# Kernel optimization log

Measured on AMD Instinct MI355X. Metric: run time of the kernel, lower is better.

## Reference

```python
import jax, jax.numpy as jnp
import numpy as np


def topk_sparsify(x, k):
    # keep k entries with largest |x|, zero the rest (matches TopKFunction.forward)
    _, idx = jax.lax.top_k(jnp.abs(x), k)            # [B, k]
    vals = jnp.take_along_axis(x, idx, axis=-1)      # [B, k]
    out = jnp.zeros_like(x)
    b = jnp.arange(x.shape[0])[:, None]              # [B, 1]
    return out.at[b, idx].set(vals)


def setup_inputs() -> dict:
    key = jax.random.key(0)
    k1, k2, k3 = jax.random.split(key, 3)
    B, D, L = 4096, 768, 16384
    x = jax.random.normal(k1, (B, D), dtype=jnp.float32)
    # kaiming_normal_(fan_out) -> std = sqrt(2 / latent_dim); then *= 2.0
    enc_w = jax.random.normal(k2, (L, D), dtype=jnp.float32) * (2.0 * np.sqrt(2.0 / L))
    enc_b = jnp.zeros((L,), dtype=jnp.float32)
    # torch Linear default init: uniform(-1/sqrt(fan_in), 1/sqrt(fan_in))
    bound = 1.0 / np.sqrt(L)
    dec_w = jax.random.uniform(k3, (D, L), dtype=jnp.float32, minval=-bound, maxval=bound)
    dec_b = jnp.zeros((D,), dtype=jnp.float32)
    return {"x": x, "enc_w": enc_w, "enc_b": enc_b, "dec_w": dec_w, "dec_b": dec_b, "k": 32}


def reference(x, enc_w, enc_b, dec_w, dec_b, k):
    pre = x @ enc_w.T + enc_b            # [B, L]
    latents = topk_sparsify(pre, k)      # [B, L], k-sparse per row
    recon = latents @ dec_w.T + dec_b    # [B, D]
    return (recon, latents, pre)
```

## Files before the change

### kernel.cpp

```cpp
#include <hip/hip_runtime.h>
#include <hip/hip_bf16.h>
#include <stdint.h>


typedef __attribute__((ext_vector_type(8))) short bf16x8;
typedef __attribute__((ext_vector_type(4))) float f32x4;

__device__ __forceinline__ ushort f2bf_rne(float v) {
    unsigned u = __float_as_uint(v);
    return (ushort)((u + 0x7fffu + ((u >> 16) & 1u)) >> 16);
}
__device__ __forceinline__ float bf2f(ushort h) {
    return __uint_as_float(((unsigned)h) << 16);
}

__global__ __launch_bounds__(256)
void prep_all(const float* __restrict__ x, const float* __restrict__ enc_w,
              const float* __restrict__ dec_w,
              ushort* __restrict__ Ah, ushort* __restrict__ Wh,
              ushort* __restrict__ WTb,
              int nA, int nW, int KT, int K, int D, int L)
{
    __shared__ float tile[32][33];
    const int bid = blockIdx.x;
    if (bid < nA + nW) {
        const float* X;
        ushort* P;
        int base;
        if (bid < nA) { X = x;     P = Ah; base = bid; }
        else          { X = enc_w; P = Wh; base = bid - nA; }
        int t = base * 256 + threadIdx.x;
        int lane = t & 63;
        int rest = t >> 6;
        int r16 = rest / KT, kt = rest - r16 * KT;
        int row = (r16 << 4) + (lane & 15);
        int k0  = (kt << 5) + ((lane >> 4) << 3);
        const float* src = X + (size_t)row * K + k0;
        uint hw[4];
        #pragma unroll
        for (int i = 0; i < 4; ++i) {
            float v0 = src[2 * i], v1 = src[2 * i + 1];
            hw[i] = (uint)f2bf_rne(v0) | ((uint)f2bf_rne(v1) << 16);
        }
        *reinterpret_cast<uint4*>(P + (size_t)t * 8) = make_uint4(hw[0], hw[1], hw[2], hw[3]);
    } else {
        int tb = bid - nA - nW;
        int gx = L >> 5;
        int l0 = (tb % gx) << 5;
        int d0 = (tb / gx) << 5;
        int tx = threadIdx.x & 31;
        int ty = threadIdx.x >> 5;
        for (int i = ty; i < 32; i += 8)
            tile[i][tx] = dec_w[(size_t)(d0 + i) * L + (l0 + tx)];
        __syncthreads();
        for (int i = ty; i < 32; i += 8)
            WTb[(size_t)(l0 + i) * D + (d0 + tx)] = f2bf_rne(tile[tx][i]);
    }
}

__global__ __launch_bounds__(256, 4)
void encoder_mfma1(const ushort* __restrict__ Ah, const ushort* __restrict__ Wh,
                   const float* __restrict__ bias, float* __restrict__ C,
                   int M, int N, int K)
{
    __shared__ ushort lds[2][8192];
    const int KT = K >> 5;
    const int tid  = threadIdx.x;
    const int lane = tid & 63;
    const int wid  = tid >> 6;

    const int gy    = M >> 7;
    const int rpx   = gy >> 3;
    const int xcd   = blockIdx.x & 7;
    const int local = blockIdx.x >> 3;
    const int by    = xcd * rpx + (local % rpx);
    const int bx    = local / rpx;

    const int wr = wid >> 1, wc = wid & 1;

    f32x4 acc[4][4];
    #pragma unroll
    for (int m = 0; m < 4; ++m)
        #pragma unroll
        for (int n = 0; n < 4; ++n) acc[m][n] = (f32x4){0.f, 0.f, 0.f, 0.f};

    auto STAGE = [&](int buf, int kt) {
        #pragma unroll
        for (int c0 = 0; c0 < 4; ++c0) {
            int c   = (wid << 2) + c0;
            int fr  = c & 7;
            int rb  = ((c < 8) ? (by << 3) : (bx << 3)) + fr;
            const ushort* g = ((c < 8) ? Ah : Wh) + (((size_t)rb * KT + kt) * 64 + lane) * 8;
            ushort* dst = &lds[buf][c * 512];
            __builtin_amdgcn_global_load_lds(
                (const __attribute__((address_space(1))) unsigned int*)g,
                (__attribute__((address_space(3))) unsigned int*)dst, 16, 0, 0);
        }
    };

    STAGE(0, 0);
    __syncthreads();

    int cur = 0;
    for (int kt = 0; kt < KT; ++kt) {
        if (kt + 1 < KT) STAGE(cur ^ 1, kt + 1);

        bf16x8 ah[4], bh[4];
        #pragma unroll
        for (int m = 0; m < 4; ++m)
            ah[m] = *reinterpret_cast<const bf16x8*>(&lds[cur][((wr << 2) + m) * 512 + lane * 8]);
        #pragma unroll
        for (int n = 0; n < 4; ++n)
            bh[n] = *reinterpret_cast<const bf16x8*>(&lds[cur][4096 + ((wc << 2) + n) * 512 + lane * 8]);

        #pragma unroll
        for (int m = 0; m < 4; ++m)
            #pragma unroll
            for (int n = 0; n < 4; ++n)
                acc[m][n] = __builtin_amdgcn_mfma_f32_16x16x32_bf16(ah[m], bh[n], acc[m][n], 0, 0, 0);

        __syncthreads();
        cur ^= 1;
    }

    const int r_in = (lane >> 4) << 2;
    const int c_in = lane & 15;
    #pragma unroll
    for (int n = 0; n < 4; ++n) {
        const int gc = (bx << 7) + (wc << 6) + (n << 4) + c_in;
        const float bv = bias[gc];
        #pragma unroll
        for (int m = 0; m < 4; ++m) {
            const int gr0 = (by << 7) + (wr << 6) + (m << 4) + r_in;
            #pragma unroll
            for (int q = 0; q < 4; ++q)
                __builtin_nontemporal_store(acc[m][n][q] + bv,
                                            &C[(size_t)(gr0 + q) * N + gc]);
        }
    }
}

#define SR_CAP 1024
#define SR_ZCAP 128

__global__ __launch_bounds__(256, 8)
void select_refine(const float* __restrict__ pre, const float* __restrict__ x,
                   const float* __restrict__ enc_w, const float* __restrict__ enc_b,
                   float* __restrict__ latents, int* __restrict__ sel_idx,
                   float* __restrict__ sel_val, const int* __restrict__ kptr,
                   const ushort* __restrict__ WT, const float* __restrict__ dbias,
                   float* __restrict__ recon, int D, int L)
{
    const int b   = blockIdx.x;
    const int tid = threadIdx.x;
    const float* row = pre + (size_t)b * L;
    float* lrow = latents + (size_t)b * L;

    __shared__ float    xs[768];
    __shared__ float    smp[256];
    __shared__ float    sthr[3];
    __shared__ int      cnt;
    __shared__ unsigned long long lkey[SR_CAP];
    __shared__ float    lval[SR_CAP];
    __shared__ float    s_tk;
    __shared__ float    s_xn2;
    __shared__ int      zidx[SR_ZCAP];
    __shared__ float    zval[SR_ZCAP];
    __shared__ int      zn;
    __shared__ int      fin_n;
    __shared__ int      fin_i[64];
    __shared__ float    fin_v[64];
    __shared__ float    red[4];

    int k = *kptr; if (k > 64) k = 64; if (k < 1) k = 1;

    float xn2p = 0.f;
    for (int i = tid; i < D; i += 256) {
        float v = x[(size_t)b * D + i];
        xs[i] = v;
        xn2p = fmaf(v, v, xn2p);
    }
    #pragma unroll
    for (int off = 32; off > 0; off >>= 1) xn2p += __shfl_down(xn2p, off);
    if ((tid & 63) == 0) red[tid >> 6] = xn2p;
    if (tid == 0) { zn = 0; fin_n = 0; }
    __syncthreads();
    if (tid == 0) s_xn2 = red[0] + red[1] + red[2] + red[3];

    const int stride = L >> 8;
    smp[tid] = fabsf(row[(size_t)tid * stride]);
    __syncthreads();
    {
        float s = smp[tid];
        int r = 0;
        for (int j = 0; j < 256; ++j) {
            float o = smp[j];
            r += (o > s || (o == s && j < tid)) ? 1 : 0;
        }
        if (r == 1) sthr[0] = s;
        if (r == 3) sthr[1] = s;
        if (r == 7) sthr[2] = s;
    }
    __syncthreads();

    float t = sthr[1];
    int n = 0;
    for (int attempt = 0; attempt < 2; ++attempt) {
        __syncthreads();
        if (tid == 0) cnt = 0;
        __syncthreads();
        for (int i = tid * 4; i < L; i += 1024) {
            f32x4 v = __builtin_nontemporal_load(
                reinterpret_cast<const f32x4*>(row + i));
            float vv[4] = {v.x, v.y, v.z, v.w};
            #pragma unroll
            for (int j = 0; j < 4; ++j) {
                float av = fabsf(vv[j]);
                if (av >= t) {
                    int p = atomicAdd(&cnt, 1);
                    if (p < SR_CAP) {
                        lkey[p] = ((unsigned long long)__float_as_uint(av) << 32)
                                  | (unsigned)(~(i + j));
                        lval[p] = vv[j];
                    }
                }
            }
        }
        __syncthreads();
        n = cnt;
        if (n >= 48 && n <= SR_CAP) break;
        t = (n < 48) ? sthr[2] : sthr[0];
    }
    if (n > SR_CAP) n = SR_CAP;
    if (k > n) k = n;

    const f32x4 z4 = (f32x4){0.f, 0.f, 0.f, 0.f};
    for (int i = tid * 4; i < L; i += 1024)
        __builtin_nontemporal_store(z4, reinterpret_cast<f32x4*>(lrow + i));

    for (int i = tid; i < n; i += 256) {
        unsigned long long ki = lkey[i];
        int rk = 0;
        for (int j = 0; j < n; ++j) rk += (lkey[j] > ki) ? 1 : 0;
        if (rk == k - 1) s_tk = fabsf(lval[i]);
    }
    __syncthreads();

    const float tk = s_tk;
    const float m  = 1.2e-3f * sqrtf(s_xn2);

    for (int i = tid; i < n; i += 256) {
        float a = fabsf(lval[i]);
        if (a > tk + m) {
            int p = atomicAdd(&fin_n, 1);
            fin_i[p] = (int)(~(unsigned)lkey[i]);
            fin_v[p] = lval[i];
        } else if (a >= tk - m) {
            int zp = atomicAdd(&zn, 1);
            if (zp < SR_ZCAP) zidx[zp] = (int)(~(unsigned)lkey[i]);
        }
    }
    __syncthreads();
    const int A  = fin_n;
    const int nz = (zn < SR_ZCAP) ? zn : SR_ZCAP;

    for (int z = 0; z < nz; ++z) {
        const int l = zidx[z];
        const float* wrow = enc_w + (size_t)l * D;
        float s = 0.f;
        for (int d = tid; d < D; d += 256) s = fmaf(xs[d], wrow[d], s);
        #pragma unroll
        for (int off = 32; off > 0; off >>= 1) s += __shfl_down(s, off);
        if ((tid & 63) == 0) red[tid >> 6] = s;
        __syncthreads();
        if (tid == 0) zval[z] = red[0] + red[1] + red[2] + red[3] + enc_b[l];
        __syncthreads();
    }

    const int k2 = k - A;
    if (tid < nz) {
        float az = fabsf(zval[tid]);
        int   iz = zidx[tid];
        int rz = 0;
        for (int j = 0; j < nz; ++j) {
            float aj = fabsf(zval[j]);
            rz += (aj > az || (aj == az && zidx[j] < iz)) ? 1 : 0;
        }
        if (rz < k2) {
            int p = atomicAdd(&fin_n, 1);
            if (p < 64) { fin_i[p] = iz; fin_v[p] = zval[tid]; }
        }
    }
    __syncthreads();

    int fn = fin_n; if (fn > 64) fn = 64;
    if (tid < fn) {
        float av = fabsf(fin_v[tid]);
        int   ii = fin_i[tid];
        int fr = 0;
        for (int j = 0; j < fn; ++j) {
            float aj = fabsf(fin_v[j]);
            fr += (aj > av || (aj == av && fin_i[j] < ii)) ? 1 : 0;
        }
        sel_idx[(size_t)b * 64 + fr] = ii;
        sel_val[(size_t)b * 64 + fr] = fin_v[tid];
        lrow[ii] = fin_v[tid];
    }
    if (tid >= fn && tid < k) {
        sel_idx[(size_t)b * 64 + tid] = 0;
        sel_val[(size_t)b * 64 + tid] = 0.f;
    }
    __syncthreads();

    float a0 = 0.f, a1 = 0.f, a2 = 0.f;
    for (int j = 0; j < fn; ++j) {
        const ushort* w = WT + (size_t)fin_i[j] * D;
        const float v = fin_v[j];
        if (tid < D)        a0 = fmaf(v, bf2f(w[tid]),       a0);
        if (tid + 256 < D)  a1 = fmaf(v, bf2f(w[tid + 256]), a1);
        if (tid + 512 < D)  a2 = fmaf(v, bf2f(w[tid + 512]), a2);
    }
    if (tid < D)
        __builtin_nontemporal_store(a0 + dbias[tid],       &recon[(size_t)b * D + tid]);
    if (tid + 256 < D)
        __builtin_nontemporal_store(a1 + dbias[tid + 256], &recon[(size_t)b * D + tid + 256]);
    if (tid + 512 < D)
        __builtin_nontemporal_store(a2 + dbias[tid + 512], &recon[(size_t)b * D + tid + 512]);
}

#define BM 128
#define BN 128
#define BKT 16

__global__ __launch_bounds__(256, 2)
void encoder_gemm(const float* __restrict__ A, const float* __restrict__ Bw,
                  const float* __restrict__ bias, float* __restrict__ C,
                  int M, int N, int K)
{
    __shared__ float As[BKT][BM + 4];
    __shared__ float Bs[BKT][BN + 4];
    const int tid  = threadIdx.x;
    const int row0 = blockIdx.y * BM;
    const int col0 = blockIdx.x * BN;
    const int lrow = tid >> 2;
    const int lc4  = (tid & 3) * 4;
    const int ty = tid >> 4;
    const int tx = tid & 15;
    float acc[2][2][4][4];
    #pragma unroll
    for (int a = 0; a < 2; ++a)
        #pragma unroll
        for (int b = 0; b < 2; ++b)
            #pragma unroll
            for (int i = 0; i < 4; ++i)
                #pragma unroll
                for (int j = 0; j < 4; ++j) acc[a][b][i][j] = 0.f;
    for (int k0 = 0; k0 < K; k0 += BKT) {
        float4 a0 = *reinterpret_cast<const float4*>(A + (size_t)(row0 + lrow)      * K + k0 + lc4);
        float4 a1 = *reinterpret_cast<const float4*>(A + (size_t)(row0 + lrow + 64) * K + k0 + lc4);
        float4 b0 = *reinterpret_cast<const float4*>(Bw + (size_t)(col0 + lrow)      * K + k0 + lc4);
        float4 b1 = *reinterpret_cast<const float4*>(Bw + (size_t)(col0 + lrow + 64) * K + k0 + lc4);
        __syncthreads();
        As[lc4 + 0][lrow] = a0.x; As[lc4 + 1][lrow] = a0.y;
        As[lc4 + 2][lrow] = a0.z; As[lc4 + 3][lrow] = a0.w;
        As[lc4 + 0][lrow + 64] = a1.x; As[lc4 + 1][lrow + 64] = a1.y;
        As[lc4 + 2][lrow + 64] = a1.z; As[lc4 + 3][lrow + 64] = a1.w;
        Bs[lc4 + 0][lrow] = b0.x; Bs[lc4 + 1][lrow] = b0.y;
        Bs[lc4 + 2][lrow] = b0.z; Bs[lc4 + 3][lrow] = b0.w;
        Bs[lc4 + 0][lrow + 64] = b1.x; Bs[lc4 + 1][lrow + 64] = b1.y;
        Bs[lc4 + 2][lrow + 64] = b1.z; Bs[lc4 + 3][lrow + 64] = b1.w;
        __syncthreads();
        #pragma unroll
        for (int kk = 0; kk < BKT; ++kk) {
            float av[2][4], bv[2][4];
            *reinterpret_cast<float4*>(av[0]) = *reinterpret_cast<const float4*>(&As[kk][ty * 4]);
            *reinterpret_cast<float4*>(av[1]) = *reinterpret_cast<const float4*>(&As[kk][ty * 4 + 64]);
            *reinterpret_cast<float4*>(bv[0]) = *reinterpret_cast<const float4*>(&Bs[kk][tx * 4]);
            *reinterpret_cast<float4*>(bv[1]) = *reinterpret_cast<const float4*>(&Bs[kk][tx * 4 + 64]);
            #pragma unroll
            for (int a = 0; a < 2; ++a)
                #pragma unroll
                for (int i = 0; i < 4; ++i)
                    #pragma unroll
                    for (int b = 0; b < 2; ++b)
                        #pragma unroll
                        for (int j = 0; j < 4; ++j)
                            acc[a][b][i][j] = fmaf(av[a][i], bv[b][j], acc[a][b][i][j]);
        }
    }
    #pragma unroll
    for (int a = 0; a < 2; ++a)
        #pragma unroll
        for (int i = 0; i < 4; ++i) {
            const int r = row0 + a * 64 + ty * 4 + i;
            #pragma unroll
            for (int b = 0; b < 2; ++b) {
                const int c = col0 + b * 64 + tx * 4;
                float4 o;
                o.x = acc[a][b][i][0] + bias[c + 0];
                o.y = acc[a][b][i][1] + bias[c + 1];
                o.z = acc[a][b][i][2] + bias[c + 2];
                o.w = acc[a][b][i][3] + bias[c + 3];
                *reinterpret_cast<float4*>(C + (size_t)r * N + c) = o;
            }
        }
}

__global__ __launch_bounds__(256)
void topk_kernel(const float* __restrict__ pre, float* __restrict__ latents,
                 const int* __restrict__ kptr, int L)
{
    const int b   = blockIdx.x;
    const int tid = threadIdx.x;
    int k = *kptr; if (k > 64) k = 64; if (k < 1) k = 1;
    const float* row = pre + (size_t)b * L;
    __shared__ unsigned hist[2048];
    __shared__ unsigned coarse[256];
    __shared__ unsigned sh_cgt, sh_prefix;
    __shared__ int      tie_n;
    __shared__ int      tie_idx[1024];
    __shared__ float    tie_val[1024];
    unsigned cgt = 0, prefix = 0;
    for (int level = 0; level < 3; ++level) {
        const int nb     = (level == 0) ? 2048 : 1024;
        const int shift  = (level == 0) ? 20 : (level == 1 ? 10 : 0);
        const int pshift = (level == 1) ? 20 : 10;
        for (int i = tid; i < nb; i += 256) hist[i] = 0;
        __syncthreads();
        for (int i = tid * 4; i < L; i += 1024) {
            float4 v = *reinterpret_cast<const float4*>(row + i);
            float vv[4] = {v.x, v.y, v.z, v.w};
            #pragma unroll
            for (int j = 0; j < 4; ++j) {
                unsigned key = __float_as_uint(vv[j]) & 0x7fffffffu;
                if (level == 0 || (key >> pshift) == prefix)
                    atomicAdd(&hist[(key >> shift) & (nb - 1)], 1u);
            }
        }
        __syncthreads();
        const int per = nb / 256;
        unsigned s = 0;
        for (int j = 0; j < per; ++j) s += hist[tid * per + j];
        coarse[tid] = s;
        __syncthreads();
        if (tid == 0) {
            unsigned run = cgt;
            int bin = 0;
            for (int c = 255; c >= 0; --c) {
                if (run + coarse[c] >= (unsigned)k) {
                    bin = c * per + per - 1;
                    for (; bin > c * per; --bin) {
                        if (run + hist[bin] >= (unsigned)k) break;
                        run += hist[bin];
                    }
                    break;
                }
                run += coarse[c];
            }
            sh_cgt = run;
            sh_prefix = (level == 0) ? (unsigned)bin : ((prefix << 10) | (unsigned)bin);
        }
        __syncthreads();
        cgt = sh_cgt; prefix = sh_prefix;
        __syncthreads();
    }
    const unsigned T = prefix;
    const int r = k - (int)cgt;
    if (tid == 0) tie_n = 0;
    __syncthreads();
    float* lrow = latents + (size_t)b * L;
    for (int i = tid * 4; i < L; i += 1024) {
        float4 v = *reinterpret_cast<const float4*>(row + i);
        float vv[4] = {v.x, v.y, v.z, v.w};
        #pragma unroll
        for (int j = 0; j < 4; ++j) {
            unsigned key = __float_as_uint(vv[j]) & 0x7fffffffu;
            if (key > T) {
                lrow[i + j] = vv[j];
            } else if (key == T) {
                int p = atomicAdd(&tie_n, 1);
                if (p < 1024) { tie_idx[p] = i + j; tie_val[p] = vv[j]; }
            }
        }
    }
    __syncthreads();
    if (tid == 0) {
        int nn = tie_n; if (nn > 1024) nn = 1024;
        for (int a = 1; a < nn; ++a) {
            int ia = tie_idx[a]; float va = tie_val[a];
            int c = a - 1;
            while (c >= 0 && tie_idx[c] > ia) {
                tie_idx[c + 1] = tie_idx[c]; tie_val[c + 1] = tie_val[c]; --c;
            }
            tie_idx[c + 1] = ia; tie_val[c + 1] = va;
        }
        int take = r < nn ? r : nn;
        for (int a = 0; a < take; ++a) lrow[tie_idx[a]] = tie_val[a];
    }
}

__global__ void transpose_kernel(const float* __restrict__ W, float* __restrict__ WT,
                                 int D, int L)
{
    __shared__ float tile[32][33];
    const int l0 = blockIdx.x * 32;
    const int d0 = blockIdx.y * 32;
    const int tx = threadIdx.x;
    const int ty = threadIdx.y;
    for (int i = ty; i < 32; i += 8)
        tile[i][tx] = W[(size_t)(d0 + i) * L + (l0 + tx)];
    __syncthreads();
    for (int i = ty; i < 32; i += 8)
        WT[(size_t)(l0 + i) * D + (d0 + tx)] = tile[tx][i];
}

__global__ __launch_bounds__(256)
void decoder_kernel(const float* __restrict__ latents, const float* __restrict__ WT,
                    const float* __restrict__ Wfall, const float* __restrict__ dbias,
                    float* __restrict__ recon, int L, int D, int useWT)
{
    const int b = blockIdx.x;
    const int tid = threadIdx.x;
    __shared__ int   nsel;
    __shared__ int   s_idx[64];
    __shared__ float s_val[64];
    if (tid == 0) nsel = 0;
    __syncthreads();
    const float* lrow = latents + (size_t)b * L;
    for (int i = tid * 4; i < L; i += 1024) {
        float4 v = *reinterpret_cast<const float4*>(lrow + i);
        float vv[4] = {v.x, v.y, v.z, v.w};
        #pragma unroll
        for (int j = 0; j < 4; ++j) {
            if (vv[j] != 0.0f) {
                int p = atomicAdd(&nsel, 1);
                if (p < 64) { s_idx[p] = i + j; s_val[p] = vv[j]; }
            }
        }
    }
    __syncthreads();
    if (tid == 0) {
        int n = nsel; if (n > 64) n = 64;
        for (int a = 1; a < n; ++a) {
            int ia = s_idx[a]; float va = s_val[a];
            int c = a - 1;
            while (c >= 0 && s_idx[c] > ia) {
                s_idx[c + 1] = s_idx[c]; s_val[c + 1] = s_val[c]; --c;
            }
            s_idx[c + 1] = ia; s_val[c + 1] = va;
        }
    }
    __syncthreads();
    int n = nsel; if (n > 64) n = 64;
    float accv[3] = {0.f, 0.f, 0.f};
    if (useWT) {
        for (int j = 0; j < n; ++j) {
            const int l = s_idx[j]; const float v = s_val[j];
            const float* w = WT + (size_t)l * D;
            #pragma unroll
            for (int c = 0; c < 3; ++c) {
                int d = tid + c * 256;
                if (d < D) accv[c] = fmaf(v, w[d], accv[c]);
            }
        }
    } else {
        for (int j = 0; j < n; ++j) {
            const int l = s_idx[j]; const float v = s_val[j];
            #pragma unroll
            for (int c = 0; c < 3; ++c) {
                int d = tid + c * 256;
                if (d < D) accv[c] = fmaf(v, Wfall[(size_t)d * L + l], accv[c]);
            }
        }
    }
    #pragma unroll
    for (int c = 0; c < 3; ++c) {
        int d = tid + c * 256;
        if (d < D) recon[(size_t)b * D + d] = accv[c] + dbias[d];
    }
}

extern "C" void kernel_launch(void* const* d_in, const int* in_sizes, int n_in,
                              void* d_out, int out_size, void* d_ws, size_t ws_size,
                              hipStream_t stream)
{
    const float* x     = (const float*)d_in[0];
    const float* enc_w = (const float*)d_in[1];
    const float* enc_b = (const float*)d_in[2];
    const float* dec_w = (const float*)d_in[3];
    const float* dec_b = (const float*)d_in[4];
    const int*   kptr  = (const int*)d_in[5];

    const int D = in_sizes[4];
    const int L = in_sizes[2];
    const int B = in_sizes[0] / D;

    float* recon   = (float*)d_out;
    float* latents = recon + (size_t)B * D;
    float* pre     = latents + (size_t)B * L;

    const size_t szA  = (size_t)B * D * 2;
    const size_t szW  = (size_t)L * D * 2;
    const size_t szSel = (size_t)B * 64 * 4;
    size_t off = 0;
    ushort* Ah  = (ushort*)((char*)d_ws + off); off += szA;
    ushort* Wh  = (ushort*)((char*)d_ws + off); off += szW;
    ushort* WTb = (ushort*)((char*)d_ws + off); off += szW;
    int*    sidx = (int*)((char*)d_ws + off);   off += szSel;
    float*  sval = (float*)((char*)d_ws + off); off += szSel;
    const size_t need = off;

    const bool shapes_ok = (B % 1024 == 0) && (L % 1024 == 0) && (L >= 2048) &&
                           (D % 32 == 0) && (D <= 768);
    const bool fast = shapes_ok && ws_size >= need;

    if (fast) {
        const int KT = D / 32;
        const int nA = (B / 16) * KT * 64 / 256;
        const int nW = (L / 16) * KT * 64 / 256;
        const int nT = (L / 32) * (D / 32);
        prep_all<<<nA + nW + nT, 256, 0, stream>>>(x, enc_w, dec_w, Ah, Wh, WTb,
                                                   nA, nW, KT, D, D, L);
        encoder_mfma1<<<(B / 128) * (L / 128), 256, 0, stream>>>(Ah, Wh, enc_b, pre, B, L, D);
        select_refine<<<B, 256, 0, stream>>>(pre, x, enc_w, enc_b, latents, sidx, sval,
                                             kptr, WTb, dec_b, recon, D, L);
    } else {
        hipMemsetAsync(latents, 0, (size_t)B * L * sizeof(float), stream);
        int useWT = 0;
        const size_t szWT = (size_t)L * D * 4;
        if (ws_size >= szWT) {
            useWT = 1;
            transpose_kernel<<<dim3(L / 32, D / 32), dim3(32, 8), 0, stream>>>(dec_w, (float*)d_ws, D, L);
        }
        encoder_gemm<<<dim3(L / BN, B / BM), 256, 0, stream>>>(x, enc_w, enc_b, pre, B, L, D);
        topk_kernel<<<B, 256, 0, stream>>>(pre, latents, kptr, L);
        decoder_kernel<<<B, 256, 0, stream>>>(latents, (float*)d_ws, dec_w, dec_b, recon, L, D, useWT);
    }
}
```

Measured before the change: 430.2 us.

## Emit top-k candidates from encoder epilogue to skip rescanning pre rows

Computes a per-row statistical threshold from ||x|| and the Frobenius norm of enc_w, then has the encoder GEMM epilogue append entries above it to a per-row global candidate list via atomics. select_refine ranks these candidates directly instead of sampling the row and streaming all of pre again. It falls back to the full scan when the count is out of range or the k-th candidate sits too close to the threshold. This adds global atomics in the GEMM epilogue, an extra small kernel, two memsets, and a small candidate workspace.

```diff
diff --git a/kernel.cpp b/kernel.cpp
--- a/kernel.cpp
+++ b/kernel.cpp
@@ -5,6 +5,8 @@
 
 typedef __attribute__((ext_vector_type(8))) short bf16x8;
 typedef __attribute__((ext_vector_type(4))) float f32x4;
+
+#define CAND_CAP 512
 
 __device__ __forceinline__ ushort f2bf_rne(float v) {
     unsigned u = __float_as_uint(v);
@@ -18,17 +20,16 @@
 void prep_all(const float* __restrict__ x, const float* __restrict__ enc_w,
               const float* __restrict__ dec_w,
               ushort* __restrict__ Ah, ushort* __restrict__ Wh,
-              ushort* __restrict__ WTb,
+              ushort* __restrict__ WTb, float* __restrict__ ss,
               int nA, int nW, int KT, int K, int D, int L)
 {
     __shared__ float tile[32][33];
     const int bid = blockIdx.x;
     if (bid < nA + nW) {
-        const float* X;
-        ushort* P;
-        int base;
-        if (bid < nA) { X = x;     P = Ah; base = bid; }
-        else          { X = enc_w; P = Wh; base = bid - nA; }
+        const bool isW = (bid >= nA);
+        const float* X = isW ? enc_w : x;
+        ushort* P = isW ? Wh : Ah;
+        int base = isW ? (bid - nA) : bid;
         int t = base * 256 + threadIdx.x;
         int lane = t & 63;
         int rest = t >> 6;
@@ -37,12 +38,19 @@
         int k0  = (kt << 5) + ((lane >> 4) << 3);
         const float* src = X + (size_t)row * K + k0;
         uint hw[4];
+        float sq = 0.f;
         #pragma unroll
         for (int i = 0; i < 4; ++i) {
             float v0 = src[2 * i], v1 = src[2 * i + 1];
+            sq = fmaf(v0, v0, sq); sq = fmaf(v1, v1, sq);
             hw[i] = (uint)f2bf_rne(v0) | ((uint)f2bf_rne(v1) << 16);
         }
         *reinterpret_cast<uint4*>(P + (size_t)t * 8) = make_uint4(hw[0], hw[1], hw[2], hw[3]);
+        if (isW) {
+            #pragma unroll
+            for (int off = 32; off > 0; off >>= 1) sq += __shfl_down(sq, off);
+            if ((threadIdx.x & 63) == 0) atomicAdd(ss, sq);
+        }
     } else {
         int tb = bid - nA - nW;
         int gx = L >> 5;
@@ -58,12 +66,29 @@
     }
 }
 
+__global__ __launch_bounds__(256)
+void row_thr(const float* __restrict__ x, const float* __restrict__ ss,
+             float* __restrict__ thr, int D, int LD_total)
+{
+    int row  = blockIdx.x * 4 + (threadIdx.x >> 6);
+    int lane = threadIdx.x & 63;
+    const float* xr = x + (size_t)row * D;
+    float s = 0.f;
+    for (int d = lane; d < D; d += 64) { float v = xr[d]; s = fmaf(v, v, s); }
+    #pragma unroll
+    for (int off = 32; off > 0; off >>= 1) s += __shfl_down(s, off);
+    if (lane == 0)
+        thr[row] = 2.5f * sqrtf(ss[0] / (float)LD_total) * sqrtf(s);
+}
+
 __global__ __launch_bounds__(256, 4)
 void encoder_mfma1(const ushort* __restrict__ Ah, const ushort* __restrict__ Wh,
                    const float* __restrict__ bias, float* __restrict__ C,
-                   int M, int N, int K)
+                   uint2* __restrict__ cand, int* __restrict__ cnt,
+                   const float* __restrict__ thr, int M, int N, int K)
 {
     __shared__ ushort lds[2][8192];
+    __shared__ float  thr_s[128];
     const int KT = K >> 5;
     const int tid  = threadIdx.x;
     const int lane = tid & 63;
@@ -77,6 +102,8 @@
     const int bx    = local / rpx;
 
     const int wr = wid >> 1, wc = wid & 1;
+
+    if (tid < 128) thr_s[tid] = thr[(by << 7) + tid];
 
     f32x4 acc[4][4];
     #pragma unroll
@@ -131,11 +158,20 @@
         const float bv = bias[gc];
         #pragma unroll
         for (int m = 0; m < 4; ++m) {
-            const int gr0 = (by << 7) + (wr << 6) + (m << 4) + r_in;
-            #pragma unroll
-            for (int q = 0; q < 4; ++q)
-                __builtin_nontemporal_store(acc[m][n][q] + bv,
-                                            &C[(size_t)(gr0 + q) * N + gc]);
+            const int lr0 = (wr << 6) + (m << 4) + r_in;
+            #pragma unroll
+            for (int q = 0; q < 4; ++q) {
+                const int lr = lr0 + q;
+                const int gr = (by << 7) + lr;
+                const float v = acc[m][n][q] + bv;
+                __builtin_nontemporal_store(v, &C[(size_t)gr * N + gc]);
+                if (fabsf(v) >= thr_s[lr]) {
+                    int p = atomicAdd(&cnt[gr], 1);
+                    if (p < CAND_CAP)
+                        cand[(size_t)gr * CAND_CAP + p] =
+                            make_uint2((unsigned)gc, __float_as_uint(v));
+                }
+            }
         }
     }
 }
@@ -146,6 +182,8 @@
 __global__ __launch_bounds__(256, 8)
 void select_refine(const float* __restrict__ pre, const float* __restrict__ x,
                    const float* __restrict__ enc_w, const float* __restrict__ enc_b,
+                   const uint2* __restrict__ cand, const int* __restrict__ cnt,
+                   const float* __restrict__ thr,
                    float* __restrict__ latents, int* __restrict__ sel_idx,
                    float* __restrict__ sel_val, const int* __restrict__ kptr,
                    const ushort* __restrict__ WT, const float* __restrict__ dbias,
@@ -159,7 +197,7 @@
     __shared__ float    xs[768];
     __shared__ float    smp[256];
     __shared__ float    sthr[3];
-    __shared__ int      cnt;
+    __shared__ int      scnt;
     __shared__ unsigned long long lkey[SR_CAP];
     __shared__ float    lval[SR_CAP];
     __shared__ float    s_tk;
@@ -187,67 +225,93 @@
     __syncthreads();
     if (tid == 0) s_xn2 = red[0] + red[1] + red[2] + red[3];
 
-    const int stride = L >> 8;
-    smp[tid] = fabsf(row[(size_t)tid * stride]);
-    __syncthreads();
-    {
-        float s = smp[tid];
-        int r = 0;
-        for (int j = 0; j < 256; ++j) {
-            float o = smp[j];
-            r += (o > s || (o == s && j < tid)) ? 1 : 0;
-        }
-        if (r == 1) sthr[0] = s;
-        if (r == 3) sthr[1] = s;
-        if (r == 7) sthr[2] = s;
-    }
-    __syncthreads();
-
-    float t = sthr[1];
+    const int nc = cnt[b];
+    bool usecand = (nc >= k && nc <= CAND_CAP);
     int n = 0;
-    for (int attempt = 0; attempt < 2; ++attempt) {
-        __syncthreads();
-        if (tid == 0) cnt = 0;
-        __syncthreads();
-        for (int i = tid * 4; i < L; i += 1024) {
-            f32x4 v = __builtin_nontemporal_load(
-                reinterpret_cast<const f32x4*>(row + i));
-            float vv[4] = {v.x, v.y, v.z, v.w};
-            #pragma unroll
-            for (int j = 0; j < 4; ++j) {
-                float av = fabsf(vv[j]);
-                if (av >= t) {
-                    int p = atomicAdd(&cnt, 1);
-                    if (p < SR_CAP) {
-                        lkey[p] = ((unsigned long long)__float_as_uint(av) << 32)
-                                  | (unsigned)(~(i + j));
-                        lval[p] = vv[j];
-                    }
-                }
-            }
-        }
-        __syncthreads();
-        n = cnt;
-        if (n >= 48 && n <= SR_CAP) break;
-        t = (n < 48) ? sthr[2] : sthr[0];
-    }
-    if (n > SR_CAP) n = SR_CAP;
-    if (k > n) k = n;
+    if (usecand) {
+        for (int i = tid; i < nc; i += 256) {
+            uint2 e = cand[(size_t)b * CAND_CAP + i];
+            lval[i] = __uint_as_float(e.y);
+            lkey[i] = ((unsigned long long)(e.y & 0x7fffffffu) << 32)
+                      | (unsigned)(~e.x);
+        }
+        n = nc;
+    }
 
     const f32x4 z4 = (f32x4){0.f, 0.f, 0.f, 0.f};
     for (int i = tid * 4; i < L; i += 1024)
         __builtin_nontemporal_store(z4, reinterpret_cast<f32x4*>(lrow + i));
-
-    for (int i = tid; i < n; i += 256) {
-        unsigned long long ki = lkey[i];
-        int rk = 0;
-        for (int j = 0; j < n; ++j) rk += (lkey[j] > ki) ? 1 : 0;
-        if (rk == k - 1) s_tk = fabsf(lval[i]);
-    }
-    __syncthreads();
-
+    __syncthreads();
+
+    const float mm   = 1.2e-3f * sqrtf(s_xn2);
+    const float thrb = thr[b];
+    int kk = 0;
+
+    for (int pass = 0; pass < 2; ++pass) {
+        if (!usecand) {
+            const int stride = L >> 8;
+            smp[tid] = fabsf(row[(size_t)tid * stride]);
+            __syncthreads();
+            {
+                float s = smp[tid];
+                int r = 0;
+                for (int j = 0; j < 256; ++j) {
+                    float o = smp[j];
+                    r += (o > s || (o == s && j < tid)) ? 1 : 0;
+                }
+                if (r == 1) sthr[0] = s;
+                if (r == 3) sthr[1] = s;
+                if (r == 7) sthr[2] = s;
+            }
+            __syncthreads();
+            float t = sthr[1];
+            for (int attempt = 0; attempt < 2; ++attempt) {
+                __syncthreads();
+                if (tid == 0) scnt = 0;
+                __syncthreads();
+                for (int i = tid * 4; i < L; i += 1024) {
+                    f32x4 v = __builtin_nontemporal_load(
+                        reinterpret_cast<const f32x4*>(row + i));
+                    float vv[4] = {v.x, v.y, v.z, v.w};
+                    #pragma unroll
+                    for (int j = 0; j < 4; ++j) {
+                        float av = fabsf(vv[j]);
+                        if (av >= t) {
+                            int p = atomicAdd(&scnt, 1);
+                            if (p < SR_CAP) {
+                                lkey[p] = ((unsigned long long)__float_as_uint(av) << 32)
+                                          | (unsigned)(~(i + j));
+                                lval[p] = vv[j];
+                            }
+                        }
+                    }
+                }
+                __syncthreads();
+                n = scnt;
+                if (n >= 48 && n <= SR_CAP) break;
+                t = (n < 48) ? sthr[2] : sthr[0];
+            }
+            if (n > SR_CAP) n = SR_CAP;
+        }
+        kk = (k < n) ? k : n;
+
+        if (tid == 0) s_tk = 0.f;
+        __syncthreads();
+        for (int i = tid; i < n; i += 256) {
+            unsigned long long ki = lkey[i];
+            int rk = 0;
+            for (int j = 0; j < n; ++j) rk += (lkey[j] > ki) ? 1 : 0;
+            if (rk == kk - 1) s_tk = fabsf(lval[i]);
+        }
+        __syncthreads();
+
+        if (!usecand) break;
+        if (s_tk >= thrb + 2.0f * mm) break;
+        usecand = false;
+    }
+    k = kk;
     const float tk = s_tk;
-    const float m  = 1.2e-3f * sqrtf(s_xn2);
+    const float m  = mm;
 
     for (int i = tid; i < n; i += 256) {
         float a = fabsf(lval[i]);
@@ -608,6 +672,10 @@
     ushort* WTb = (ushort*)((char*)d_ws + off); off += szW;
     int*    sidx = (int*)((char*)d_ws + off);   off += szSel;
     float*  sval = (float*)((char*)d_ws + off); off += szSel;
+    uint2*  candb = (uint2*)((char*)d_ws + off); off += (size_t)B * CAND_CAP * 8;
+    int*    cntb  = (int*)((char*)d_ws + off);   off += (size_t)B * 4;
+    float*  thrb  = (float*)((char*)d_ws + off); off += (size_t)B * 4;
+    float*  ssb   = (float*)((char*)d_ws + off); off += 256;
     const size_t need = off;
 
     const bool shapes_ok = (B % 1024 == 0) && (L % 1024 == 0) && (L >= 2048) &&
@@ -619,11 +687,16 @@
         const int nA = (B / 16) * KT * 64 / 256;
         const int nW = (L / 16) * KT * 64 / 256;
         const int nT = (L / 32) * (D / 32);
-        prep_all<<<nA + nW + nT, 256, 0, stream>>>(x, enc_w, dec_w, Ah, Wh, WTb,
+        hipMemsetAsync(cntb, 0, (size_t)B * 4, stream);
+        hipMemsetAsync(ssb, 0, 4, stream);
+        prep_all<<<nA + nW + nT, 256, 0, stream>>>(x, enc_w, dec_w, Ah, Wh, WTb, ssb,
                                                    nA, nW, KT, D, D, L);
-        encoder_mfma1<<<(B / 128) * (L / 128), 256, 0, stream>>>(Ah, Wh, enc_b, pre, B, L, D);
-        select_refine<<<B, 256, 0, stream>>>(pre, x, enc_w, enc_b, latents, sidx, sval,
-                                             kptr, WTb, dec_b, recon, D, L);
+        row_thr<<<B / 4, 256, 0, stream>>>(x, ssb, thrb, D, L * D);
+        encoder_mfma1<<<(B / 128) * (L / 128), 256, 0, stream>>>(
+            Ah, Wh, enc_b, pre, candb, cntb, thrb, B, L, D);
+        select_refine<<<B, 256, 0, stream>>>(
+            pre, x, enc_w, enc_b, candb, cntb, thrb, latents, sidx, sval,
+            kptr, WTb, dec_b, recon, D, L);
     } else {
         hipMemsetAsync(latents, 0, (size_t)B * L * sizeof(float), stream);
         int useWT = 0;
```

New measurement: 716.3 us. 66.5% more time.
